# Performance work log

Hardware: AMD Instinct MI355X
Metric: run time of the kernel (lower is better)

## Reference

```python
import jax, jax.numpy as jnp
import numpy as np

E = 8      # num_experts
K = 2      # top-k
DIM = 1024
DFF = 2048  # fused gate+up width; intermediate = DFF // 2 == DIM


def setup_inputs() -> dict:
    key = jax.random.key(0)
    ks = jax.random.split(key, 5)
    B, S = 4, 2048
    x = jax.random.normal(ks[0], (B, S, DIM), dtype=jnp.float32)
    Wg = jax.random.normal(ks[1], (E, DIM), dtype=jnp.float32) * 0.02
    bg = jax.random.normal(ks[2], (E,), dtype=jnp.float32) * 0.02
    w1 = jax.random.normal(ks[3], (E, DFF, DIM), dtype=jnp.float32) * 0.02
    w2 = jax.random.normal(ks[4], (E, DIM, DFF // 2), dtype=jnp.float32) * 0.02
    return {"x": x, "Wg": Wg, "bg": bg, "w1": w1, "w2": w2}


def _moe(x, Wg, bg, w1, w2):
    B, S, D = x.shape
    t = x.reshape(-1, D)                      # [T, D] tokens
    logits = t @ Wg.T + bg                    # [T, E]
    probs = jax.nn.softmax(logits, axis=-1)
    topw, topi = jax.lax.top_k(probs, K)      # [T, K]
    topw = topw / jnp.sum(topw, axis=-1, keepdims=True)  # renormalize=True
    # per-token combine weight for each expert (0 if not selected): [T, E]
    combine = jnp.sum(jax.nn.one_hot(topi, E, dtype=t.dtype) * topw[..., None], axis=1)

    def body(acc, packed):
        w1e, w2e, ce = packed                 # [DFF, D], [D, DFF//2], [T]
        h = t @ w1e.T                         # [T, DFF]
        gate, up = jnp.split(h, 2, axis=-1)   # silu_and_mul (SwiGLU)
        a = jax.nn.silu(gate) * up            # [T, DFF//2]
        o = a @ w2e.T                         # [T, D]
        return acc + ce[:, None] * o, None

    out, _ = jax.lax.scan(body, jnp.zeros_like(t), (w1, w2, combine.T))
    return out.reshape(B, S, D)


def reference(x, Wg, bg, w1, w2):
    return _moe(x, Wg, bg, w1, w2)
```

## Files before the change

### kernel.cpp

```cpp
#include <hip/hip_runtime.h>
#include <hip/hip_bf16.h>
#include <cstdint>

#define T_TOKENS 8192
#define DIM 1024
#define NEXP 8
#define DFFH 1024
#define ROWCAP 17408
#define NCHUNK 16
#define MAXMT 24

typedef __attribute__((ext_vector_type(8))) short bf16x8;
typedef __attribute__((ext_vector_type(4))) float f32x4;
typedef __attribute__((ext_vector_type(16))) float f32x16;

__device__ __forceinline__ ushort f2bf(float f) {
  uint32_t u = __float_as_uint(f);
  uint32_t r = (u + 0x7fffu + ((u >> 16) & 1u)) >> 16;
  return (ushort)r;
}
__device__ __forceinline__ float bf2f(ushort u) {
  return __uint_as_float(((uint32_t)u) << 16);
}

__device__ __forceinline__ void async16(const void* g, const void* l) {
  __builtin_amdgcn_global_load_lds(
      (const __attribute__((address_space(1))) void*)(uintptr_t)g,
      (__attribute__((address_space(3))) void*)(uintptr_t)l, 16, 0, 0);
}

__global__ __launch_bounds__(256) void cast_kernel(
    const float4* __restrict__ w1, const float4* __restrict__ w2,
    ushort* __restrict__ w1b, ushort* __restrict__ w2b) {
  const int NW1 = NEXP * 2048 * DIM / 4;
  const int NW2 = NEXP * DIM * DFFH / 4;
  const int total = NW1 + NW2;
  for (int i = blockIdx.x * 256 + threadIdx.x; i < total; i += 2048 * 256) {
    float4 v; ushort* dst;
    if (i < NW1) { v = w1[i]; dst = w1b + (size_t)i * 4; }
    else { int j = i - NW1; v = w2[j]; dst = w2b + (size_t)j * 4; }
    ushort4 o4;
    o4.x = f2bf(v.x); o4.y = f2bf(v.y); o4.z = f2bf(v.z); o4.w = f2bf(v.w);
    *(ushort4*)dst = o4;
  }
}

__global__ __launch_bounds__(256) void gate_kernel(
    const float4* __restrict__ x4, const float4* __restrict__ Wg4,
    const float* __restrict__ bg, int* __restrict__ top2e,
    float2* __restrict__ top2w, ushort* __restrict__ xb) {
  __shared__ float4 wgl[NEXP * 256];
  const int tid = threadIdx.x;
  for (int i = tid; i < NEXP * 256; i += 256) wgl[i] = Wg4[i];
  __syncthreads();
  const int wave = tid >> 6, lane = tid & 63;
  const float bgsel = bg[lane & 7];
  const int t0 = (blockIdx.x * 4 + wave) * 16;
  for (int tt = 0; tt < 16; ++tt) {
    const int t = t0 + tt;
    const float4* xr = x4 + (size_t)t * 256;
    ushort4* xw = (ushort4*)(xb + (size_t)t * DIM);
    float acc[NEXP];
#pragma unroll
    for (int e = 0; e < NEXP; ++e) acc[e] = 0.f;
#pragma unroll
    for (int j = 0; j < 4; ++j) {
      float4 xv = xr[lane + j * 64];
      ushort4 o4;
      o4.x = f2bf(xv.x); o4.y = f2bf(xv.y); o4.z = f2bf(xv.z); o4.w = f2bf(xv.w);
      xw[lane + j * 64] = o4;
#pragma unroll
      for (int e = 0; e < NEXP; ++e) {
        float4 wv = wgl[e * 256 + lane + j * 64];
        acc[e] += xv.x * wv.x + xv.y * wv.y + xv.z * wv.z + xv.w * wv.w;
      }
    }
#pragma unroll
    for (int e = 0; e < NEXP; ++e) {
      float v = acc[e];
      v += __shfl_xor(v, 1); v += __shfl_xor(v, 2); v += __shfl_xor(v, 4);
      acc[e] = v;
    }
    float v = acc[0];
#pragma unroll
    for (int e = 1; e < NEXP; ++e) v = ((lane & 7) == e) ? acc[e] : v;
    v += __shfl_xor(v, 8); v += __shfl_xor(v, 16); v += __shfl_xor(v, 32);
    v += bgsel;
    float m1 = v;
    m1 = fmaxf(m1, __shfl_xor(m1, 1));
    m1 = fmaxf(m1, __shfl_xor(m1, 2));
    m1 = fmaxf(m1, __shfl_xor(m1, 4));
    unsigned long long mk = __ballot(v == m1);
    int bi = (int)(__ffsll(mk) - 1) & 7;
    float v2 = (((lane & 7) == bi) ? -1e30f : v);
    float m2 = v2;
    m2 = fmaxf(m2, __shfl_xor(m2, 1));
    m2 = fmaxf(m2, __shfl_xor(m2, 2));
    m2 = fmaxf(m2, __shfl_xor(m2, 4));
    mk = __ballot(v2 == m2);
    int si = (int)(__ffsll(mk) - 1) & 7;
    if (lane == 0) {
      float w0 = 1.f / (1.f + __expf(m2 - m1));
      top2e[t] = bi | (si << 8);
      top2w[t] = make_float2(w0, 1.f - w0);
    }
  }
}

__global__ __launch_bounds__(1024) void route_kernel(
    const int* __restrict__ top2e, int* __restrict__ cnt,
    int* __restrict__ off, int* __restrict__ base ) {
  __shared__ int chunkcnt[NCHUNK][NEXP];
  const int tid = threadIdx.x;
  int c[NEXP];
#pragma unroll
  for (int e = 0; e < NEXP; ++e) c[e] = 0;
  const int4* p = (const int4*)(top2e + tid * 8);
  int4 a = p[0], b = p[1];
  int vals[8] = {a.x, a.y, a.z, a.w, b.x, b.y, b.z, b.w};
#pragma unroll
  for (int k = 0; k < 8; ++k) {
    int e0 = vals[k] & 255, e1 = (vals[k] >> 8) & 255;
#pragma unroll
    for (int e = 0; e < NEXP; ++e) c[e] += (e0 == e) + (e1 == e);
  }
#pragma unroll
  for (int e = 0; e < NEXP; ++e) {
    c[e] += __shfl_xor(c[e], 1);  c[e] += __shfl_xor(c[e], 2);
    c[e] += __shfl_xor(c[e], 4);  c[e] += __shfl_xor(c[e], 8);
    c[e] += __shfl_xor(c[e], 16); c[e] += __shfl_xor(c[e], 32);
  }
  const int wave = tid >> 6, lane = tid & 63;
  if (lane == 0) {
#pragma unroll
    for (int e = 0; e < NEXP; ++e) chunkcnt[wave][e] = c[e];
  }
  __syncthreads();
  if (tid == 0) {
    int o = 0;
    off[0] = 0;
    for (int e = 0; e < NEXP; ++e) {
      int tot = 0;
      for (int w = 0; w < NCHUNK; ++w) tot += chunkcnt[w][e];
      cnt[e] = tot;
      int run = o;
      for (int w = 0; w < NCHUNK; ++w) { base[w * NEXP + e] = run; run += chunkcnt[w][e]; }
      o += (tot + 127) & ~127;
      off[e + 1] = o;
    }
  }
}

__global__ __launch_bounds__(512) void scatter_kernel(
    const int* __restrict__ top2e, const float2* __restrict__ top2w,
    const int* __restrict__ base, int* __restrict__ rows_token,
    float* __restrict__ rows_weight, int2* __restrict__ tok2row) {
  __shared__ int lcnt[NEXP];
  const int tid = threadIdx.x;
  if (tid < NEXP) lcnt[tid] = 0;
  __syncthreads();
  const int b = blockIdx.x;
  const int t = b * 512 + tid;
  int pk = top2e[t];
  float2 w = top2w[t];
  int e0 = pk & 255, e1 = (pk >> 8) & 255;
  int p0 = atomicAdd(&lcnt[e0], 1);
  int p1 = atomicAdd(&lcnt[e1], 1);
  int r0 = base[b * NEXP + e0] + p0;
  int r1 = base[b * NEXP + e1] + p1;
  rows_token[r0] = t; rows_weight[r0] = w.x;
  rows_token[r1] = t; rows_weight[r1] = w.y;
  tok2row[t] = make_int2(r0, r1);
}

__global__ __launch_bounds__(256) void mlpA_kernel(
    const ushort* __restrict__ xb, const ushort* __restrict__ w1b,
    const int* __restrict__ rows_token, const int* __restrict__ cnt,
    const int* __restrict__ off, ushort* __restrict__ abuf) {
  const int bid = blockIdx.x;
  const int e = bid & 7;
  const int pos = bid >> 3;
  const int mt = pos >> 4, nt = pos & 15;
  const int count = cnt[e];
  if (mt * 128 >= count) return;
  const int base = off[e];

  __shared__ ushort As[2][128 * 64];
  __shared__ ushort Bs[2][2][64 * 64];

  const int tid = threadIdx.x;
  const int wave = tid >> 6, lane = tid & 63;
  const int wm = wave >> 1, wn = wave & 1;
  const int cg = tid & 7;
  const int r7w = (tid >> 3) & 7;
  const int cgs = (cg ^ r7w) * 8;

  const ushort* gA[4];
#pragma unroll
  for (int i = 0; i < 4; ++i) {
    int row = i * 32 + (tid >> 3);
    int r = mt * 128 + row;
    int tok = (r < count) ? rows_token[base + r] : 0;
    gA[i] = xb + ((size_t)tok * DIM + cgs);
  }
  const ushort* gBg[2];
  const ushort* gBu[2];
#pragma unroll
  for (int i = 0; i < 2; ++i) {
    int row = i * 32 + (tid >> 3);
    gBg[i] = w1b + ((size_t)(e * 2048 + nt * 64 + row) * DIM + cgs);
    gBu[i] = w1b + ((size_t)(e * 2048 + 1024 + nt * 64 + row) * DIM + cgs);
  }

#define STAGE_A1(b_, k0_)                                             \
  {                                                                   \
    _Pragma("unroll")                                                 \
    for (int i = 0; i < 4; ++i)                                       \
      async16(gA[i] + (k0_), &As[b_][(i * 256 + wave * 64) * 8]);     \
    _Pragma("unroll")                                                 \
    for (int i = 0; i < 2; ++i) {                                     \
      async16(gBg[i] + (k0_), &Bs[b_][0][(i * 256 + wave * 64) * 8]); \
      async16(gBu[i] + (k0_), &Bs[b_][1][(i * 256 + wave * 64) * 8]); \
    }                                                                 \
  }

  f32x16 accg0 = {0,0,0,0,0,0,0,0,0,0,0,0,0,0,0,0};
  f32x16 accg1 = accg0, accu0 = accg0, accu1 = accg0;

  const int xr = (lane & 7) << 3;
  const int la31 = lane & 31;
  const int kbase = (lane >> 5) * 8;

#define COMPA(b_)                                                              \
  {                                                                            \
    _Pragma("unroll")                                                          \
    for (int kk = 0; kk < 4; ++kk) {                                           \
      const int ko = (kk * 16 + kbase) ^ xr;                                   \
      bf16x8 a0 = *(const bf16x8*)&As[b_][(wm * 64 + la31) * 64 + ko];         \
      bf16x8 a1 = *(const bf16x8*)&As[b_][(wm * 64 + 32 + la31) * 64 + ko];    \
      bf16x8 bg_ = *(const bf16x8*)&Bs[b_][0][(wn * 32 + la31) * 64 + ko];     \
      bf16x8 bu_ = *(const bf16x8*)&Bs[b_][1][(wn * 32 + la31) * 64 + ko];     \
      accg0 = __builtin_amdgcn_mfma_f32_32x32x16_bf16(a0, bg_, accg0, 0, 0, 0);\
      accg1 = __builtin_amdgcn_mfma_f32_32x32x16_bf16(a1, bg_, accg1, 0, 0, 0);\
      accu0 = __builtin_amdgcn_mfma_f32_32x32x16_bf16(a0, bu_, accu0, 0, 0, 0);\
      accu1 = __builtin_amdgcn_mfma_f32_32x32x16_bf16(a1, bu_, accu1, 0, 0, 0);\
    }                                                                          \
  }

  STAGE_A1(0, 0);
  __syncthreads();
#pragma unroll
  for (int it = 0; it < 8; ++it) {
    STAGE_A1(1, it * 128 + 64);
    COMPA(0);
    __syncthreads();
    if (it < 7) STAGE_A1(0, it * 128 + 128);
    COMPA(1);
    __syncthreads();
  }

  const int colg = nt * 64 + wn * 32 + la31;
  const size_t rbase = (size_t)(base + mt * 128 + wm * 64);
  const int rlo = 4 * (lane >> 5);
#pragma unroll
  for (int s = 0; s < 2; ++s) {
    const f32x16 g16 = s ? accg1 : accg0;
    const f32x16 u16 = s ? accu1 : accu0;
#pragma unroll
    for (int r = 0; r < 16; ++r) {
      int rr = (r & 3) + 8 * (r >> 2) + rlo;
      float g = g16[r], u = u16[r];
      float a = (g / (1.f + __expf(-g))) * u;
      abuf[(rbase + s * 32 + rr) * DFFH + colg] = f2bf(a);
    }
  }
#undef STAGE_A1
#undef COMPA
}

__global__ __launch_bounds__(256) void mlpB_kernel(
    const ushort* __restrict__ abuf, const ushort* __restrict__ w2b,
    const float* __restrict__ rows_weight, const int* __restrict__ cnt,
    const int* __restrict__ off, ushort* __restrict__ obuf) {
  const int bid = blockIdx.x;
  const int e = bid & 7;
  const int pos = bid >> 3;
  const int mt = pos >> 3, nt = pos & 7;
  const int count = cnt[e];
  if (mt * 128 >= count) return;
  const int base = off[e];

  __shared__ ushort As[2][128 * 64];
  __shared__ ushort Bs[2][128 * 64];

  const int tid = threadIdx.x;
  const int wave = tid >> 6, lane = tid & 63;
  const int wm = wave >> 1, wn = wave & 1;
  const int cg = tid & 7;
  const int r7w = (tid >> 3) & 7;
  const int cgs = (cg ^ r7w) * 8;

  const ushort* gA[4];
#pragma unroll
  for (int i = 0; i < 4; ++i) {
    int row = i * 32 + (tid >> 3);
    gA[i] = abuf + ((size_t)(base + mt * 128 + row) * DFFH + cgs);
  }
  const ushort* gB[4];
#pragma unroll
  for (int i = 0; i < 4; ++i) {
    int row = i * 32 + (tid >> 3);
    gB[i] = w2b + ((size_t)(e * 1024 + nt * 128 + row) * DFFH + cgs);
  }

#define STAGE_B1(b_, k0_)                                           \
  {                                                                 \
    _Pragma("unroll")                                               \
    for (int i = 0; i < 4; ++i) {                                   \
      async16(gA[i] + (k0_), &As[b_][(i * 256 + wave * 64) * 8]);   \
      async16(gB[i] + (k0_), &Bs[b_][(i * 256 + wave * 64) * 8]);   \
    }                                                               \
  }

  f32x16 acc00 = {0,0,0,0,0,0,0,0,0,0,0,0,0,0,0,0};
  f32x16 acc01 = acc00, acc10 = acc00, acc11 = acc00;

  const int xr = (lane & 7) << 3;
  const int la31 = lane & 31;
  const int kbase = (lane >> 5) * 8;

#define COMPB(b_)                                                              \
  {                                                                            \
    _Pragma("unroll")                                                          \
    for (int kk = 0; kk < 4; ++kk) {                                           \
      const int ko = (kk * 16 + kbase) ^ xr;                                   \
      bf16x8 a0 = *(const bf16x8*)&As[b_][(wm * 64 + la31) * 64 + ko];         \
      bf16x8 a1 = *(const bf16x8*)&As[b_][(wm * 64 + 32 + la31) * 64 + ko];    \
      bf16x8 b0 = *(const bf16x8*)&Bs[b_][(wn * 64 + la31) * 64 + ko];         \
      bf16x8 b1 = *(const bf16x8*)&Bs[b_][(wn * 64 + 32 + la31) * 64 + ko];    \
      acc00 = __builtin_amdgcn_mfma_f32_32x32x16_bf16(a0, b0, acc00, 0, 0, 0); \
      acc01 = __builtin_amdgcn_mfma_f32_32x32x16_bf16(a0, b1, acc01, 0, 0, 0); \
      acc10 = __builtin_amdgcn_mfma_f32_32x32x16_bf16(a1, b0, acc10, 0, 0, 0); \
      acc11 = __builtin_amdgcn_mfma_f32_32x32x16_bf16(a1, b1, acc11, 0, 0, 0); \
    }                                                                          \
  }

  STAGE_B1(0, 0);
  __syncthreads();
#pragma unroll
  for (int it = 0; it < 8; ++it) {
    STAGE_B1(1, it * 128 + 64);
    COMPB(0);
    __syncthreads();
    if (it < 7) STAGE_B1(0, it * 128 + 128);
    COMPB(1);
    __syncthreads();
  }

  const int rlo = 4 * (lane >> 5);
  const int colb = nt * 128 + wn * 64 + la31;
#pragma unroll
  for (int s = 0; s < 2; ++s) {
    const f32x16 c0 = s ? acc10 : acc00;
    const f32x16 c1 = s ? acc11 : acc01;
#pragma unroll
    for (int r = 0; r < 16; ++r) {
      int rr = (r & 3) + 8 * (r >> 2) + rlo;
      int lrow = mt * 128 + wm * 64 + s * 32 + rr;
      if (lrow < count) {
        float wgt = rows_weight[base + lrow];
        obuf[(size_t)(base + lrow) * DIM + colb] = f2bf(wgt * c0[r]);
        obuf[(size_t)(base + lrow) * DIM + colb + 32] = f2bf(wgt * c1[r]);
      }
    }
  }
#undef STAGE_B1
#undef COMPB
}

__global__ __launch_bounds__(256) void combine_kernel(
    const ushort* __restrict__ obuf, const int2* __restrict__ tok2row,
    float* __restrict__ out) {
  const int t = blockIdx.x;
  int2 rr = tok2row[t];
  const ushort4* p0 = (const ushort4*)(obuf + (size_t)rr.x * DIM);
  const ushort4* p1 = (const ushort4*)(obuf + (size_t)rr.y * DIM);
  float4* po = (float4*)(out + (size_t)t * DIM);
  const int c = threadIdx.x;
  ushort4 a = p0[c], b = p1[c];
  float4 o;
  o.x = bf2f(a.x) + bf2f(b.x);
  o.y = bf2f(a.y) + bf2f(b.y);
  o.z = bf2f(a.z) + bf2f(b.z);
  o.w = bf2f(a.w) + bf2f(b.w);
  po[c] = o;
}

extern "C" void kernel_launch(void* const* d_in, const int* in_sizes, int n_in,
                              void* d_out, int out_size, void* d_ws, size_t ws_size,
                              hipStream_t stream) {
  const float* x = (const float*)d_in[0];
  const float* Wg = (const float*)d_in[1];
  const float* bg = (const float*)d_in[2];
  const float* w1 = (const float*)d_in[3];
  const float* w2 = (const float*)d_in[4];
  float* out = (float*)d_out;

  char* ws = (char*)d_ws;
  ushort* xb = (ushort*)ws;
  ushort* w1b = xb + (size_t)T_TOKENS * DIM;
  ushort* w2b = w1b + (size_t)NEXP * 2048 * DIM;
  ushort* abuf = w2b + (size_t)NEXP * DIM * DFFH;
  char* p = (char*)(abuf + (size_t)ROWCAP * DFFH);
  int* top2e = (int*)p;            p += T_TOKENS * 4;
  float2* top2w = (float2*)p;      p += T_TOKENS * 8;
  int* rows_token = (int*)p;       p += ROWCAP * 4;
  float* rows_weight = (float*)p;  p += ROWCAP * 4;
  int2* tok2row = (int2*)p;        p += T_TOKENS * 8;
  int* cnt = (int*)p;              p += 32;
  int* off = (int*)p;              p += 64;
  int* base = (int*)p;             p += NCHUNK * NEXP * 4;
  ushort* obuf = xb;

  cast_kernel<<<2048, 256, 0, stream>>>((const float4*)w1, (const float4*)w2,
                                        w1b, w2b);
  gate_kernel<<<128, 256, 0, stream>>>((const float4*)x, (const float4*)Wg, bg,
                                       top2e, top2w, xb);
  route_kernel<<<1, 1024, 0, stream>>>(top2e, cnt, off, base);
  scatter_kernel<<<NCHUNK, 512, 0, stream>>>(top2e, top2w, base, rows_token,
                                             rows_weight, tok2row);
  mlpA_kernel<<<8 * MAXMT * 16, 256, 0, stream>>>(xb, w1b, rows_token, cnt, off, abuf);
  mlpB_kernel<<<8 * MAXMT * 8, 256, 0, stream>>>(abuf, w2b, rows_weight, cnt, off, obuf);
  combine_kernel<<<T_TOKENS, 256, 0, stream>>>(obuf, tok2row, out);
}
```

Before: 250.5 us.

## Software-pipeline MoE GEMM mainloops with explicit waitcnt, barriers and MFMA priority

Both expert GEMM kernels now load all LDS fragments for a stage into registers first, then sync and immediately issue the next global-to-LDS prefetch into the same buffer. The MFMAs for the current stage run while that prefetch is in flight. Full __syncthreads are replaced with vmcnt/lgkmcnt waits, raw s_barrier and sched_barrier fences, and s_setprio raises wave priority during MFMA bursts. This is meant to keep the load in flight across the whole compute phase instead of waiting each half-iteration. It raises register pressure, and correctness depends on the hand-counted vmcnt values.

```diff
diff --git a/kernel.cpp b/kernel.cpp
--- a/kernel.cpp
+++ b/kernel.cpp
@@ -13,6 +13,11 @@
 typedef __attribute__((ext_vector_type(8))) short bf16x8;
 typedef __attribute__((ext_vector_type(4))) float f32x4;
 typedef __attribute__((ext_vector_type(16))) float f32x16;
+
+#define VMWAIT(n) asm volatile("s_waitcnt vmcnt(" #n ")" ::: "memory")
+#define LGKWAIT   asm volatile("s_waitcnt lgkmcnt(0)" ::: "memory")
+#define SBAR      __builtin_amdgcn_s_barrier()
+#define SCHEDB    __builtin_amdgcn_sched_barrier(0)
 
 __device__ __forceinline__ ushort f2bf(float f) {
   uint32_t u = __float_as_uint(f);
@@ -231,32 +236,35 @@
   const int la31 = lane & 31;
   const int kbase = (lane >> 5) * 8;
 
-#define COMPA(b_)                                                              \
-  {                                                                            \
-    _Pragma("unroll")                                                          \
-    for (int kk = 0; kk < 4; ++kk) {                                           \
-      const int ko = (kk * 16 + kbase) ^ xr;                                   \
-      bf16x8 a0 = *(const bf16x8*)&As[b_][(wm * 64 + la31) * 64 + ko];         \
-      bf16x8 a1 = *(const bf16x8*)&As[b_][(wm * 64 + 32 + la31) * 64 + ko];    \
-      bf16x8 bg_ = *(const bf16x8*)&Bs[b_][0][(wn * 32 + la31) * 64 + ko];     \
-      bf16x8 bu_ = *(const bf16x8*)&Bs[b_][1][(wn * 32 + la31) * 64 + ko];     \
-      accg0 = __builtin_amdgcn_mfma_f32_32x32x16_bf16(a0, bg_, accg0, 0, 0, 0);\
-      accg1 = __builtin_amdgcn_mfma_f32_32x32x16_bf16(a1, bg_, accg1, 0, 0, 0);\
-      accu0 = __builtin_amdgcn_mfma_f32_32x32x16_bf16(a0, bu_, accu0, 0, 0, 0);\
-      accu1 = __builtin_amdgcn_mfma_f32_32x32x16_bf16(a1, bu_, accu1, 0, 0, 0);\
-    }                                                                          \
-  }
-
   STAGE_A1(0, 0);
-  __syncthreads();
-#pragma unroll
-  for (int it = 0; it < 8; ++it) {
-    STAGE_A1(1, it * 128 + 64);
-    COMPA(0);
-    __syncthreads();
-    if (it < 7) STAGE_A1(0, it * 128 + 128);
-    COMPA(1);
-    __syncthreads();
+  STAGE_A1(1, 64);
+  VMWAIT(8); SCHEDB; SBAR; SCHEDB;
+
+#pragma unroll
+  for (int t = 0; t < 16; ++t) {
+    const int b = t & 1;
+    bf16x8 fa0[4], fa1[4], fbg[4], fbu[4];
+#pragma unroll
+    for (int kk = 0; kk < 4; ++kk) {
+      const int ko = (kk * 16 + kbase) ^ xr;
+      fa0[kk] = *(const bf16x8*)&As[b][(wm * 64 + la31) * 64 + ko];
+      fa1[kk] = *(const bf16x8*)&As[b][(wm * 64 + 32 + la31) * 64 + ko];
+      fbg[kk] = *(const bf16x8*)&Bs[b][0][(wn * 32 + la31) * 64 + ko];
+      fbu[kk] = *(const bf16x8*)&Bs[b][1][(wn * 32 + la31) * 64 + ko];
+    }
+    LGKWAIT; SCHEDB; SBAR; SCHEDB;
+    if (t < 14) STAGE_A1(b, t * 64 + 128);
+    __builtin_amdgcn_s_setprio(1);
+#pragma unroll
+    for (int kk = 0; kk < 4; ++kk) {
+      accg0 = __builtin_amdgcn_mfma_f32_32x32x16_bf16(fa0[kk], fbg[kk], accg0, 0, 0, 0);
+      accg1 = __builtin_amdgcn_mfma_f32_32x32x16_bf16(fa1[kk], fbg[kk], accg1, 0, 0, 0);
+      accu0 = __builtin_amdgcn_mfma_f32_32x32x16_bf16(fa0[kk], fbu[kk], accu0, 0, 0, 0);
+      accu1 = __builtin_amdgcn_mfma_f32_32x32x16_bf16(fa1[kk], fbu[kk], accu1, 0, 0, 0);
+    }
+    __builtin_amdgcn_s_setprio(0);
+    if (t < 14)       { VMWAIT(8); SCHEDB; SBAR; SCHEDB; }
+    else if (t == 14) { VMWAIT(0); SCHEDB; SBAR; SCHEDB; }
   }
 
   const int colg = nt * 64 + wn * 32 + la31;
@@ -275,7 +283,6 @@
     }
   }
 #undef STAGE_A1
-#undef COMPA
 }
 
 __global__ __launch_bounds__(256) void mlpB_kernel(
@@ -329,32 +336,35 @@
   const int la31 = lane & 31;
   const int kbase = (lane >> 5) * 8;
 
-#define COMPB(b_)                                                              \
-  {                                                                            \
-    _Pragma("unroll")                                                          \
-    for (int kk = 0; kk < 4; ++kk) {                                           \
-      const int ko = (kk * 16 + kbase) ^ xr;                                   \
-      bf16x8 a0 = *(const bf16x8*)&As[b_][(wm * 64 + la31) * 64 + ko];         \
-      bf16x8 a1 = *(const bf16x8*)&As[b_][(wm * 64 + 32 + la31) * 64 + ko];    \
-      bf16x8 b0 = *(const bf16x8*)&Bs[b_][(wn * 64 + la31) * 64 + ko];         \
-      bf16x8 b1 = *(const bf16x8*)&Bs[b_][(wn * 64 + 32 + la31) * 64 + ko];    \
-      acc00 = __builtin_amdgcn_mfma_f32_32x32x16_bf16(a0, b0, acc00, 0, 0, 0); \
-      acc01 = __builtin_amdgcn_mfma_f32_32x32x16_bf16(a0, b1, acc01, 0, 0, 0); \
-      acc10 = __builtin_amdgcn_mfma_f32_32x32x16_bf16(a1, b0, acc10, 0, 0, 0); \
-      acc11 = __builtin_amdgcn_mfma_f32_32x32x16_bf16(a1, b1, acc11, 0, 0, 0); \
-    }                                                                          \
-  }
-
   STAGE_B1(0, 0);
-  __syncthreads();
-#pragma unroll
-  for (int it = 0; it < 8; ++it) {
-    STAGE_B1(1, it * 128 + 64);
-    COMPB(0);
-    __syncthreads();
-    if (it < 7) STAGE_B1(0, it * 128 + 128);
-    COMPB(1);
-    __syncthreads();
+  STAGE_B1(1, 64);
+  VMWAIT(8); SCHEDB; SBAR; SCHEDB;
+
+#pragma unroll
+  for (int t = 0; t < 16; ++t) {
+    const int b = t & 1;
+    bf16x8 fa0[4], fa1[4], fb0[4], fb1[4];
+#pragma unroll
+    for (int kk = 0; kk < 4; ++kk) {
+      const int ko = (kk * 16 + kbase) ^ xr;
+      fa0[kk] = *(const bf16x8*)&As[b][(wm * 64 + la31) * 64 + ko];
+      fa1[kk] = *(const bf16x8*)&As[b][(wm * 64 + 32 + la31) * 64 + ko];
+      fb0[kk] = *(const bf16x8*)&Bs[b][(wn * 64 + la31) * 64 + ko];
+      fb1[kk] = *(const bf16x8*)&Bs[b][(wn * 64 + 32 + la31) * 64 + ko];
+    }
+    LGKWAIT; SCHEDB; SBAR; SCHEDB;
+    if (t < 14) STAGE_B1(b, t * 64 + 128);
+    __builtin_amdgcn_s_setprio(1);
+#pragma unroll
+    for (int kk = 0; kk < 4; ++kk) {
+      acc00 = __builtin_amdgcn_mfma_f32_32x32x16_bf16(fa0[kk], fb0[kk], acc00, 0, 0, 0);
+      acc01 = __builtin_amdgcn_mfma_f32_32x32x16_bf16(fa0[kk], fb1[kk], acc01, 0, 0, 0);
+      acc10 = __builtin_amdgcn_mfma_f32_32x32x16_bf16(fa1[kk], fb0[kk], acc10, 0, 0, 0);
+      acc11 = __builtin_amdgcn_mfma_f32_32x32x16_bf16(fa1[kk], fb1[kk], acc11, 0, 0, 0);
+    }
+    __builtin_amdgcn_s_setprio(0);
+    if (t < 14)       { VMWAIT(8); SCHEDB; SBAR; SCHEDB; }
+    else if (t == 14) { VMWAIT(0); SCHEDB; SBAR; SCHEDB; }
   }
 
   const int rlo = 4 * (lane >> 5);
@@ -375,7 +385,6 @@
     }
   }
 #undef STAGE_B1
-#undef COMPB
 }
 
 __global__ __launch_bounds__(256) void combine_kernel(
```

Result: slower. 260.6 us (+4.1%).

## Fuse weight cast into gate kernel and fold routing counts into scatter

Applied to the files above, without the earlier changes.

Merges the weight-cast and gate kernels into a single launch in which the first 128 blocks do gating and the remaining blocks cast the weights, so the two run concurrently. The gate blocks now also write per-block expert counts. The scatter kernel derives totals, offsets and per-chunk bases from those counts, which removes the single-block route kernel. This cuts two launches and a serial one-block stage. In exchange, every scatter block redundantly reduces the count table.

```diff
diff --git a/kernel.cpp b/kernel.cpp
--- a/kernel.cpp
+++ b/kernel.cpp
@@ -9,9 +9,10 @@
 #define ROWCAP 17408
 #define NCHUNK 16
 #define MAXMT 24
+#define NGATEB 128
+#define NCASTB 1920
 
 typedef __attribute__((ext_vector_type(8))) short bf16x8;
-typedef __attribute__((ext_vector_type(4))) float f32x4;
 typedef __attribute__((ext_vector_type(16))) float f32x16;
 
 __device__ __forceinline__ ushort f2bf(float f) {
@@ -29,29 +30,35 @@
       (__attribute__((address_space(3))) void*)(uintptr_t)l, 16, 0, 0);
 }
 
-__global__ __launch_bounds__(256) void cast_kernel(
-    const float4* __restrict__ w1, const float4* __restrict__ w2,
-    ushort* __restrict__ w1b, ushort* __restrict__ w2b) {
-  const int NW1 = NEXP * 2048 * DIM / 4;
-  const int NW2 = NEXP * DIM * DFFH / 4;
-  const int total = NW1 + NW2;
-  for (int i = blockIdx.x * 256 + threadIdx.x; i < total; i += 2048 * 256) {
-    float4 v; ushort* dst;
-    if (i < NW1) { v = w1[i]; dst = w1b + (size_t)i * 4; }
-    else { int j = i - NW1; v = w2[j]; dst = w2b + (size_t)j * 4; }
-    ushort4 o4;
-    o4.x = f2bf(v.x); o4.y = f2bf(v.y); o4.z = f2bf(v.z); o4.w = f2bf(v.w);
-    *(ushort4*)dst = o4;
-  }
-}
-
-__global__ __launch_bounds__(256) void gate_kernel(
+__global__ __launch_bounds__(256) void gatecast_kernel(
     const float4* __restrict__ x4, const float4* __restrict__ Wg4,
-    const float* __restrict__ bg, int* __restrict__ top2e,
-    float2* __restrict__ top2w, ushort* __restrict__ xb) {
+    const float* __restrict__ bg, const float4* __restrict__ w1,
+    const float4* __restrict__ w2, int* __restrict__ top2e,
+    float2* __restrict__ top2w, ushort* __restrict__ xb,
+    ushort* __restrict__ w1b, ushort* __restrict__ w2b,
+    int* __restrict__ blkcnt ) {
   __shared__ float4 wgl[NEXP * 256];
+  __shared__ int lcnt[NEXP];
   const int tid = threadIdx.x;
+
+  if (blockIdx.x >= NGATEB) {
+    const int NW1 = NEXP * 2048 * DIM / 4;
+    const int NW2 = NEXP * DIM * DFFH / 4;
+    const int total = NW1 + NW2;
+    const int cb = blockIdx.x - NGATEB;
+    for (int i = cb * 256 + tid; i < total; i += NCASTB * 256) {
+      float4 v; ushort* dst;
+      if (i < NW1) { v = w1[i]; dst = w1b + (size_t)i * 4; }
+      else { int j = i - NW1; v = w2[j]; dst = w2b + (size_t)j * 4; }
+      ushort4 o4;
+      o4.x = f2bf(v.x); o4.y = f2bf(v.y); o4.z = f2bf(v.z); o4.w = f2bf(v.w);
+      *(ushort4*)dst = o4;
+    }
+    return;
+  }
+
   for (int i = tid; i < NEXP * 256; i += 256) wgl[i] = Wg4[i];
+  if (tid < NEXP) lcnt[tid] = 0;
   __syncthreads();
   const int wave = tid >> 6, lane = tid & 63;
   const float bgsel = bg[lane & 7];
@@ -103,71 +110,60 @@
       float w0 = 1.f / (1.f + __expf(m2 - m1));
       top2e[t] = bi | (si << 8);
       top2w[t] = make_float2(w0, 1.f - w0);
-    }
-  }
-}
-
-__global__ __launch_bounds__(1024) void route_kernel(
-    const int* __restrict__ top2e, int* __restrict__ cnt,
-    int* __restrict__ off, int* __restrict__ base ) {
-  __shared__ int chunkcnt[NCHUNK][NEXP];
+      atomicAdd(&lcnt[bi], 1);
+      atomicAdd(&lcnt[si], 1);
+    }
+  }
+  __syncthreads();
+  if (tid < NEXP) blkcnt[blockIdx.x * NEXP + tid] = lcnt[tid];
+}
+
+__global__ __launch_bounds__(512) void scatter_kernel(
+    const int* __restrict__ top2e, const float2* __restrict__ top2w,
+    const int* __restrict__ blkcnt, int* __restrict__ rows_token,
+    float* __restrict__ rows_weight, int2* __restrict__ tok2row,
+    int* __restrict__ cnt, int* __restrict__ off) {
+  __shared__ int s_all[NGATEB * NEXP];
+  __shared__ int s_tot[NEXP], s_pre[NEXP];
+  __shared__ int s_base[NEXP];
+  __shared__ int lcnt[NEXP];
   const int tid = threadIdx.x;
-  int c[NEXP];
-#pragma unroll
-  for (int e = 0; e < NEXP; ++e) c[e] = 0;
-  const int4* p = (const int4*)(top2e + tid * 8);
-  int4 a = p[0], b = p[1];
-  int vals[8] = {a.x, a.y, a.z, a.w, b.x, b.y, b.z, b.w};
-#pragma unroll
-  for (int k = 0; k < 8; ++k) {
-    int e0 = vals[k] & 255, e1 = (vals[k] >> 8) & 255;
-#pragma unroll
-    for (int e = 0; e < NEXP; ++e) c[e] += (e0 == e) + (e1 == e);
-  }
-#pragma unroll
-  for (int e = 0; e < NEXP; ++e) {
-    c[e] += __shfl_xor(c[e], 1);  c[e] += __shfl_xor(c[e], 2);
-    c[e] += __shfl_xor(c[e], 4);  c[e] += __shfl_xor(c[e], 8);
-    c[e] += __shfl_xor(c[e], 16); c[e] += __shfl_xor(c[e], 32);
-  }
-  const int wave = tid >> 6, lane = tid & 63;
-  if (lane == 0) {
-#pragma unroll
-    for (int e = 0; e < NEXP; ++e) chunkcnt[wave][e] = c[e];
+  const int b = blockIdx.x;
+  s_all[tid] = blkcnt[tid];
+  s_all[512 + tid] = blkcnt[512 + tid];
+  if (tid < NEXP) lcnt[tid] = 0;
+  __syncthreads();
+  if (tid < NEXP) {
+    int tot = 0, pre = 0;
+    const int cutoff = b * (NGATEB / NCHUNK);
+#pragma unroll 1
+    for (int k = 0; k < NGATEB; ++k) {
+      int v = s_all[k * NEXP + tid];
+      tot += v;
+      if (k < cutoff) pre += v;
+    }
+    s_tot[tid] = tot; s_pre[tid] = pre;
   }
   __syncthreads();
   if (tid == 0) {
     int o = 0;
-    off[0] = 0;
+#pragma unroll
     for (int e = 0; e < NEXP; ++e) {
-      int tot = 0;
-      for (int w = 0; w < NCHUNK; ++w) tot += chunkcnt[w][e];
-      cnt[e] = tot;
-      int run = o;
-      for (int w = 0; w < NCHUNK; ++w) { base[w * NEXP + e] = run; run += chunkcnt[w][e]; }
-      o += (tot + 127) & ~127;
-      off[e + 1] = o;
-    }
-  }
-}
-
-__global__ __launch_bounds__(512) void scatter_kernel(
-    const int* __restrict__ top2e, const float2* __restrict__ top2w,
-    const int* __restrict__ base, int* __restrict__ rows_token,
-    float* __restrict__ rows_weight, int2* __restrict__ tok2row) {
-  __shared__ int lcnt[NEXP];
-  const int tid = threadIdx.x;
-  if (tid < NEXP) lcnt[tid] = 0;
-  __syncthreads();
-  const int b = blockIdx.x;
+      s_base[e] = o + s_pre[e];
+      if (b == 0) { cnt[e] = s_tot[e]; off[e] = o; }
+      o += (s_tot[e] + 127) & ~127;
+    }
+    if (b == 0) off[NEXP] = o;
+  }
+  __syncthreads();
   const int t = b * 512 + tid;
   int pk = top2e[t];
   float2 w = top2w[t];
   int e0 = pk & 255, e1 = (pk >> 8) & 255;
   int p0 = atomicAdd(&lcnt[e0], 1);
   int p1 = atomicAdd(&lcnt[e1], 1);
-  int r0 = base[b * NEXP + e0] + p0;
-  int r1 = base[b * NEXP + e1] + p1;
+  int r0 = s_base[e0] + p0;
+  int r1 = s_base[e1] + p1;
   rows_token[r0] = t; rows_weight[r0] = w.x;
   rows_token[r1] = t; rows_weight[r1] = w.y;
   tok2row[t] = make_int2(r0, r1);
@@ -419,16 +415,14 @@
   int2* tok2row = (int2*)p;        p += T_TOKENS * 8;
   int* cnt = (int*)p;              p += 32;
   int* off = (int*)p;              p += 64;
-  int* base = (int*)p;             p += NCHUNK * NEXP * 4;
+  int* blkcnt = (int*)p;           p += NGATEB * NEXP * 4;
   ushort* obuf = xb;
 
-  cast_kernel<<<2048, 256, 0, stream>>>((const float4*)w1, (const float4*)w2,
-                                        w1b, w2b);
-  gate_kernel<<<128, 256, 0, stream>>>((const float4*)x, (const float4*)Wg, bg,
-                                       top2e, top2w, xb);
-  route_kernel<<<1, 1024, 0, stream>>>(top2e, cnt, off, base);
-  scatter_kernel<<<NCHUNK, 512, 0, stream>>>(top2e, top2w, base, rows_token,
-                                             rows_weight, tok2row);
+  gatecast_kernel<<<NGATEB + NCASTB, 256, 0, stream>>>(
+      (const float4*)x, (const float4*)Wg, bg, (const float4*)w1,
+      (const float4*)w2, top2e, top2w, xb, w1b, w2b, blkcnt);
+  scatter_kernel<<<NCHUNK, 512, 0, stream>>>(top2e, top2w, blkcnt, rows_token,
+                                             rows_weight, tok2row, cnt, off);
   mlpA_kernel<<<8 * MAXMT * 16, 256, 0, stream>>>(xb, w1b, rows_token, cnt, off, abuf);
   mlpB_kernel<<<8 * MAXMT * 8, 256, 0, stream>>>(abuf, w2b, rows_weight, cnt, off, obuf);
   combine_kernel<<<T_TOKENS, 256, 0, stream>>>(obuf, tok2row, out);
```

After: 231.6 us (median of 2 runs). 7.5% less time.
